# Kernel optimization log

Measured on AMD Instinct MI355X. Metric: run time of the kernel, lower is better.

Reference implementation:

```python
import jax, jax.numpy as jnp
import numpy as np
import math

CR = 16  # compress_ratio


def _head_mlp(x, W1, b1, W2, b2):
    # x: [..., NH, DH, CR]; per-head timm-style Mlp CR -> 4*CR -> 1 with exact GELU
    h = jax.nn.gelu(jnp.einsum('bgmnhk,nkf->bgmnhf', x, W1) + b1[:, None, :], approximate=False)
    return jnp.einsum('bgmnhf,nfo->bgmnho', h, W2) + b2[:, None, :]


def setup_inputs() -> dict:
    key = jax.random.key(0)
    ks = jax.random.split(key, 8)
    B, L, T, D, NH, OUT = 2, 256, 250, 1024, 16, 1024
    HID = 4 * CR
    mem = jax.random.normal(ks[0], (B, L * T + 1, D), jnp.float32)
    lm_emb = jax.random.normal(ks[1], (B, L, 1, D), jnp.float32)  # only shape is used
    dim_pe = jax.random.normal(ks[2], (CR, D), jnp.float32) * 0.02
    s1 = 1.0 / math.sqrt(CR)
    s2 = 1.0 / math.sqrt(HID)
    vW1 = jax.random.normal(ks[3], (NH, CR, HID), jnp.float32) * s1
    vb1 = jnp.zeros((NH, HID), jnp.float32)
    vW2 = jax.random.normal(ks[4], (NH, HID, 1), jnp.float32) * s2
    vb2 = jnp.zeros((NH, 1), jnp.float32)
    hW1 = jax.random.normal(ks[5], (NH, CR, HID), jnp.float32) * s1
    hb1 = jnp.zeros((NH, HID), jnp.float32)
    hW2 = jax.random.normal(ks[6], (NH, HID, 1), jnp.float32) * s2
    hb2 = jnp.zeros((NH, 1), jnp.float32)
    projW = jax.random.normal(ks[7], (OUT, D), jnp.float32) * (1.0 / math.sqrt(D))
    projb = jnp.zeros((OUT,), jnp.float32)
    return dict(mem=mem, lm_emb=lm_emb, dim_pe=dim_pe,
                vW1=vW1, vb1=vb1, vW2=vW2, vb2=vb2,
                hW1=hW1, hb1=hb1, hW2=hW2, hb2=hb2,
                projW=projW, projb=projb)


def reference(mem, lm_emb, dim_pe, vW1, vb1, vW2, vb2, hW1, hb1, hW2, hb2, projW, projb):
    B, L, _, D = lm_emb.shape
    NH = vW1.shape[0]
    DH = D // NH
    nonsense = mem[:, -1:]                                 # [B,1,D]
    x = mem[:, :-1].reshape(B, L, -1, D)                   # [B,L,T,D]
    T = x.shape[2]
    CL = L // CR
    # vertical compression over l-groups of CR
    v = jnp.transpose(x, (0, 2, 1, 3)).reshape(B, T, CL, CR, NH, DH)
    v = v + dim_pe.reshape(1, 1, 1, CR, NH, DH)
    v = jnp.transpose(v, (0, 1, 2, 4, 5, 3))               # [B,T,CL,NH,DH,CR]
    v = _head_mlp(v, vW1, vb1, vW2, vb2)[..., 0]           # [B,T,CL,NH,DH]
    v = v.reshape(B, T, CL, D)
    v = jnp.transpose(v, (0, 2, 1, 3))                     # [B,CL,T,D]
    # pad t to a multiple of CR with the 'nonsense' token
    pad_t = -(-T // CR) * CR
    pad = jnp.broadcast_to(nonsense.reshape(B, 1, 1, D), (B, CL, pad_t - T, D))
    v = jnp.concatenate([v, pad], axis=-2)                 # [B,CL,pad_t,D]
    # horizontal compression over t-groups of CR
    h = v.reshape(B, CL, pad_t // CR, CR, NH, DH)
    h = jnp.transpose(h, (0, 1, 2, 4, 5, 3))               # [B,CL,pad_t//CR,NH,DH,CR]
    h = _head_mlp(h, hW1, hb1, hW2, hb2)[..., 0]           # [B,CL,pad_t//CR,NH,DH]
    h = h.reshape(B, CL * (pad_t // CR), D)
    return h @ projW.T + projb
```

## Files before the change

kernel.cpp:

```cpp
#include <hip/hip_runtime.h>
#include <hip/hip_bf16.h>

#define B_ 2
#define L_ 256
#define T_ 250
#define D_ 1024
#define NH_ 16
#define DH_ 64
#define CRv_ 16
#define HID_ 64
#define CL_ 16
#define OUT_ 1024
#define MEMROWS_ 64001L

#define AS1 __attribute__((address_space(1)))
#define AS3 __attribute__((address_space(3)))

typedef __attribute__((ext_vector_type(2))) _Float16 h16x2;
typedef __attribute__((ext_vector_type(8))) _Float16 h16x8;
typedef __attribute__((ext_vector_type(4))) float f32x4;

__device__ __forceinline__ h16x2 cvt_pk(float lo, float hi) {
    return __builtin_bit_cast(h16x2, __builtin_amdgcn_cvt_pkrtz(lo, hi));
}
__device__ __forceinline__ unsigned cvt_pku(float lo, float hi) {
    return __builtin_bit_cast(unsigned, __builtin_amdgcn_cvt_pkrtz(lo, hi));
}

struct H4 { h16x2 a, b, c, d; };
__device__ __forceinline__ h16x8 packH4(h16x2 a, h16x2 b, h16x2 c, h16x2 d) {
    H4 h{a, b, c, d};
    return __builtin_bit_cast(h16x8, h);
}

__device__ __forceinline__ unsigned pk_fma(unsigned a, unsigned b, unsigned c) {
    unsigned d; asm("v_pk_fma_f16 %0, %1, %2, %3" : "=v"(d) : "v"(a), "v"(b), "v"(c)); return d;
}
__device__ __forceinline__ unsigned pk_mul(unsigned a, unsigned b) {
    unsigned d; asm("v_pk_mul_f16 %0, %1, %2" : "=v"(d) : "v"(a), "v"(b)); return d;
}
__device__ __forceinline__ unsigned pk_add(unsigned a, unsigned b) {
    unsigned d; asm("v_pk_add_f16 %0, %1, %2" : "=v"(d) : "v"(a), "v"(b)); return d;
}
__device__ __forceinline__ unsigned pk_max(unsigned a, unsigned b) {
    unsigned d; asm("v_pk_max_f16 %0, %1, %2" : "=v"(d) : "v"(a), "v"(b)); return d;
}
__device__ __forceinline__ unsigned pk_min(unsigned a, unsigned b) {
    unsigned d; asm("v_pk_min_f16 %0, %1, %2" : "=v"(d) : "v"(a), "v"(b)); return d;
}

struct GC { unsigned c0, c1, c2, c3, c4, clo, chi; };
__device__ __forceinline__ GC make_gc() {
    GC g;
    g.c0  = cvt_pku( 1.5957600f,   1.5957600f);
    g.c1  = cvt_pku(-1.0445624f,  -1.0445624f);
    g.c2  = cvt_pku( 0.5417632f,   0.5417632f);
    g.c3  = cvt_pku(-0.15817472f, -0.15817472f);
    g.c4  = cvt_pku( 0.018604288f, 0.018604288f);
    g.clo = cvt_pku(-1.75f, -1.75f);
    g.chi = cvt_pku( 1.75f,  1.75f);
    return g;
}

__device__ __forceinline__ void gelu_w2_asm(unsigned aH, unsigned w, unsigned& pacc, const GC& gc) {
    unsigned t = pk_min(pk_max(aH, gc.clo), gc.chi);
    unsigned s = pk_mul(t, t);
    unsigned p = pk_fma(gc.c4, s, gc.c3);
    p = pk_fma(p, s, gc.c2);
    p = pk_fma(p, s, gc.c1);
    p = pk_fma(p, s, gc.c0);
    unsigned e = pk_mul(t, p);
    unsigned g = pk_fma(aH, e, aH);
    pacc = pk_fma(g, w, pacc);
}

#define WAITV(n) asm volatile("s_waitcnt vmcnt(" #n ")" ::: "memory")
#define MEMBAR() asm volatile("" ::: "memory")

__global__ __launch_bounds__(512) void k_stage1(
    const float* __restrict__ mem, const float* __restrict__ dim_pe,
    const float* __restrict__ W1, const float* __restrict__ b1,
    const float* __restrict__ W2, const float* __restrict__ b2,
    _Float16* __restrict__ vbuf)
{
    extern __shared__ float stage[];

    const int blk   = blockIdx.x;
    const int dhalf = blk & 1;
    const int tch   = (blk >> 1) & 7;
    const int cl    = (blk >> 4) & 15;
    const int b     = blk >> 8;
    const int lane  = threadIdx.x & 63;
    const int wv    = threadIdx.x >> 6;
    const int nh    = dhalf * 8 + wv;
    const int g     = lane >> 4;
    const int fl    = lane & 15;
    const int kbase = (8 * g) & 15;
    const bool klive = (g < 2);

    const float* membase = mem + (long)b * MEMROWS_ * D_;
    _Float16* vrow = vbuf + (long)(b * CL_ + cl) * T_ * D_;
    const int t0   = tch * 31 + (tch < 2 ? tch : 2);
    const int tend = (tch < 2) ? 32 : 31;

    const GC gc = make_gc();

    h16x8 peq[4];
#pragma unroll
    for (int ct = 0; ct < 4; ++ct) {
        const int d0 = nh * DH_ + ct * 16 + fl;
        float p0 = dim_pe[(kbase + 0) * D_ + d0];
        float p1 = dim_pe[(kbase + 1) * D_ + d0];
        float p2 = dim_pe[(kbase + 2) * D_ + d0];
        float p3 = dim_pe[(kbase + 3) * D_ + d0];
        float p4 = dim_pe[(kbase + 4) * D_ + d0];
        float p5 = dim_pe[(kbase + 5) * D_ + d0];
        float p6 = dim_pe[(kbase + 6) * D_ + d0];
        float p7 = dim_pe[(kbase + 7) * D_ + d0];
        peq[ct] = packH4(cvt_pk(p0, p1), cvt_pk(p2, p3), cvt_pk(p4, p5), cvt_pk(p6, p7));
    }

    h16x8 bfragA[4];
    f32x4 ci[4];
    unsigned w2u[8];
#pragma unroll
    for (int cn = 0; cn < 4; ++cn) {
        h16x2 q[4];
#pragma unroll
        for (int jp = 0; jp < 4; ++jp) {
            float w0 = 0.5f * W1[(nh * CRv_ + kbase + 2 * jp + 0) * HID_ + cn * 16 + fl];
            float w1 = 0.5f * W1[(nh * CRv_ + kbase + 2 * jp + 1) * HID_ + cn * 16 + fl];
            q[jp] = cvt_pk(w0, w1);
        }
        bfragA[cn] = packH4(q[0], q[1], q[2], q[3]);
#pragma unroll
        for (int r = 0; r < 4; ++r) ci[cn][r] = 0.5f * b1[nh * HID_ + cn * 16 + 4 * g + r];
        w2u[2 * cn + 0] = cvt_pku(W2[nh * HID_ + cn * 16 + 4 * g + 0],
                                  W2[nh * HID_ + cn * 16 + 4 * g + 1]);
        w2u[2 * cn + 1] = cvt_pku(W2[nh * HID_ + cn * 16 + 4 * g + 2],
                                  W2[nh * HID_ + cn * 16 + 4 * g + 3]);
    }
    const float b2s = b2[nh];
    const unsigned b2p = cvt_pku(b2s, b2s);

    const int r0 = 2 * wv, r1 = 2 * wv + 1;
    const float* gp0 = membase + ((size_t)(cl * CRv_ + r0) * T_ + t0) * D_ + dhalf * 512 +   0 + lane * 4;
    const float* gp1 = membase + ((size_t)(cl * CRv_ + r0) * T_ + t0) * D_ + dhalf * 512 + 256 + lane * 4;
    const float* gp2 = membase + ((size_t)(cl * CRv_ + r1) * T_ + t0) * D_ + dhalf * 512 +   0 + lane * 4;
    const float* gp3 = membase + ((size_t)(cl * CRv_ + r1) * T_ + t0) * D_ + dhalf * 512 + 256 + lane * 4;

#define ISSUE(bf) do { \
    float* lb = stage + (bf) * 8192; \
    __builtin_amdgcn_global_load_lds((const AS1 void*)gp0, (AS3 void*)(lb + r0 * 512 +   0), 16, 0, 0); \
    __builtin_amdgcn_global_load_lds((const AS1 void*)gp1, (AS3 void*)(lb + r0 * 512 + 256), 16, 0, 0); \
    __builtin_amdgcn_global_load_lds((const AS1 void*)gp2, (AS3 void*)(lb + r1 * 512 +   0), 16, 0, 0); \
    __builtin_amdgcn_global_load_lds((const AS1 void*)gp3, (AS3 void*)(lb + r1 * 512 + 256), 16, 0, 0); \
    gp0 += D_; gp1 += D_; gp2 += D_; gp3 += D_; } while (0)

    ISSUE(0);

    for (int tt = 0; tt < tend; ++tt) {
        if (tt + 1 < tend) {
            ISSUE((tt + 1) & 1);
            if (tt == 0) WAITV(4); else WAITV(5);
        } else {
            WAITV(1);
        }
        __builtin_amdgcn_s_barrier();
        MEMBAR();

        const float* bufp = stage + (tt & 1) * 8192;
        float prl[4];
#pragma unroll
        for (int ct = 0; ct < 4; ++ct) {
            const int col = wv * 64 + ct * 16 + fl;
            float a0 = bufp[(kbase + 0) * 512 + col];
            float a1 = bufp[(kbase + 1) * 512 + col];
            float a2 = bufp[(kbase + 2) * 512 + col];
            float a3 = bufp[(kbase + 3) * 512 + col];
            float a4 = bufp[(kbase + 4) * 512 + col];
            float a5 = bufp[(kbase + 5) * 512 + col];
            float a6 = bufp[(kbase + 6) * 512 + col];
            float a7 = bufp[(kbase + 7) * 512 + col];
            h16x8 xq = packH4(cvt_pk(a0, a1), cvt_pk(a2, a3), cvt_pk(a4, a5), cvt_pk(a6, a7));
            h16x8 af = klive ? xq : peq[ct];

            f32x4 acc[4];
#pragma unroll
            for (int cn = 0; cn < 4; ++cn)
                acc[cn] = __builtin_amdgcn_mfma_f32_16x16x32_f16(bfragA[cn], af, ci[cn], 0, 0, 0);

            unsigned pc0 = 0u, pc1 = 0u;
#pragma unroll
            for (int cn = 0; cn < 4; ++cn) {
                unsigned a01 = cvt_pku(acc[cn][0], acc[cn][1]);
                unsigned a23 = cvt_pku(acc[cn][2], acc[cn][3]);
                gelu_w2_asm(a01, w2u[2 * cn + 0], pc0, gc);
                gelu_w2_asm(a23, w2u[2 * cn + 1], pc1, gc);
            }
            h16x2 P = __builtin_bit_cast(h16x2, pk_add(pc0, pc1));
            prl[ct] = (float)P[0] + (float)P[1];
        }

        unsigned A  = cvt_pku(prl[0], prl[1]);
        unsigned Bp = cvt_pku(prl[2], prl[3]);
        A  = pk_add(A,  (unsigned)__shfl_xor((int)A, 16));
        Bp = pk_add(Bp, (unsigned)__shfl_xor((int)Bp, 16));
        A  = pk_add(A,  (unsigned)__shfl_xor((int)A, 32));
        Bp = pk_add(Bp, (unsigned)__shfl_xor((int)Bp, 32));
        A  = pk_add(A, b2p);
        Bp = pk_add(Bp, b2p);
        unsigned sel = (g < 2) ? A : Bp;
        unsigned sh  = (g & 1) ? (sel >> 16) : sel;
        vrow[(size_t)(t0 + tt) * D_ + nh * DH_ + g * 16 + fl] =
            __builtin_bit_cast(_Float16, (unsigned short)sh);

        MEMBAR();
        __builtin_amdgcn_s_barrier();
        MEMBAR();
    }
#undef ISSUE
}

__global__ __launch_bounds__(256) void k_stage2(
    const _Float16* __restrict__ vbuf, const float* __restrict__ mem,
    const float* __restrict__ W1, const float* __restrict__ b1,
    const float* __restrict__ W2, const float* __restrict__ b2,
    _Float16* __restrict__ hbuf)
{
    const int blk = blockIdx.x;
    const int nhg = blk & 3;
    const int tc  = (blk >> 2) & 15;
    const int cl  = (blk >> 6) & 15;
    const int b   = blk >> 10;
    const int lane = threadIdx.x & 63;
    const int wv   = threadIdx.x >> 6;
    const int nh   = nhg * 4 + wv;
    const int g    = lane >> 4;
    const int fl   = lane & 15;
    const int kbase = (8 * g) & 15;
    const bool klive = (g < 2);

    const _Float16* vrow = vbuf + (long)(b * CL_ + cl) * T_ * D_;
    const float* nons = mem + ((long)b * MEMROWS_ + (long)L_ * T_) * D_;

    const GC gc = make_gc();

    h16x8 bfragA[4];
    f32x4 ci[4];
    unsigned w2u[8];
#pragma unroll
    for (int cn = 0; cn < 4; ++cn) {
        h16x2 q[4];
#pragma unroll
        for (int jp = 0; jp < 4; ++jp) {
            float w0 = 0.5f * W1[(nh * CRv_ + kbase + 2 * jp + 0) * HID_ + cn * 16 + fl];
            float w1 = 0.5f * W1[(nh * CRv_ + kbase + 2 * jp + 1) * HID_ + cn * 16 + fl];
            h16x2 qq = cvt_pk(w0, w1);
            if (!klive) { qq[0] = (_Float16)0.f; qq[1] = (_Float16)0.f; }
            q[jp] = qq;
        }
        bfragA[cn] = packH4(q[0], q[1], q[2], q[3]);
#pragma unroll
        for (int r = 0; r < 4; ++r) ci[cn][r] = 0.5f * b1[nh * HID_ + cn * 16 + 4 * g + r];
        w2u[2 * cn + 0] = cvt_pku(W2[nh * HID_ + cn * 16 + 4 * g + 0],
                                  W2[nh * HID_ + cn * 16 + 4 * g + 1]);
        w2u[2 * cn + 1] = cvt_pku(W2[nh * HID_ + cn * 16 + 4 * g + 2],
                                  W2[nh * HID_ + cn * 16 + 4 * g + 3]);
    }
    const float b2s = b2[nh];

#pragma unroll 1
    for (int ct = 0; ct < 4; ++ct) {
        const int d0 = nh * DH_ + ct * 16 + fl;
        const _Float16 nv = (_Float16)nons[d0];

        h16x2 q[4];
#pragma unroll
        for (int jp = 0; jp < 4; ++jp) {
            h16x2 qq;
#pragma unroll
            for (int e = 0; e < 2; ++e) {
                const int t   = tc * CRv_ + kbase + 2 * jp + e;
                const int tcl = (t < T_) ? t : (T_ - 1);
                _Float16 us = vrow[tcl * D_ + d0];
                qq[e] = (t < T_) ? us : nv;
            }
            q[jp] = qq;
        }
        h16x8 af = packH4(q[0], q[1], q[2], q[3]);

        f32x4 acc[4];
#pragma unroll
        for (int cn = 0; cn < 4; ++cn)
            acc[cn] = __builtin_amdgcn_mfma_f32_16x16x32_f16(bfragA[cn], af, ci[cn], 0, 0, 0);

        unsigned pc0 = 0u, pc1 = 0u;
#pragma unroll
        for (int cn = 0; cn < 4; ++cn) {
            unsigned a01 = cvt_pku(acc[cn][0], acc[cn][1]);
            unsigned a23 = cvt_pku(acc[cn][2], acc[cn][3]);
            gelu_w2_asm(a01, w2u[2 * cn + 0], pc0, gc);
            gelu_w2_asm(a23, w2u[2 * cn + 1], pc1, gc);
        }
        h16x2 P = __builtin_bit_cast(h16x2, pk_add(pc0, pc1));
        float pr = (float)P[0] + (float)P[1];
        pr += __shfl_xor(pr, 16);
        pr += __shfl_xor(pr, 32);

        if (g == 0)
            hbuf[(long)((b * CL_ + cl) * 16 + tc) * D_ + d0] = (_Float16)(pr + b2s);
    }
}

__global__ __launch_bounds__(256) void k_proj(
    const _Float16* __restrict__ H, const float* __restrict__ Wp,
    const float* __restrict__ bias, float* __restrict__ Cout)
{
    __shared__ _Float16 Ht[64][40];
    __shared__ _Float16 Wt[32][40];

    const int bn = blockIdx.x & 31;
    const int bm = blockIdx.x >> 5;
    const int tid = threadIdx.x;
    const int lane = tid & 63, wv = tid >> 6;
    const int g = lane >> 4, fl = lane & 15;
    const int m0 = bm * 64, n0 = bn * 32;

    const int hrow = tid >> 2, hko = (tid & 3) * 8;
    const int wrow = tid >> 3, wko = (tid & 7) * 4;

    const int nw  = (wv & 1) * 16;
    const int mwb = (wv >> 1) * 32;

    f32x4 acc[2] = {{0.f,0.f,0.f,0.f},{0.f,0.f,0.f,0.f}};

    for (int k0 = 0; k0 < 1024; k0 += 32) {
        uint4 hv = *reinterpret_cast<const uint4*>(&H[(size_t)(m0 + hrow) * OUT_ + k0 + hko]);
        *reinterpret_cast<uint4*>(&Ht[hrow][hko]) = hv;
        float4 wf = *reinterpret_cast<const float4*>(&Wp[(size_t)(n0 + wrow) * D_ + k0 + wko]);
        uint2 wu;
        wu.x = cvt_pku(wf.x, wf.y);
        wu.y = cvt_pku(wf.z, wf.w);
        *reinterpret_cast<uint2*>(&Wt[wrow][wko]) = wu;
        __syncthreads();

        h16x8 wfrag = *reinterpret_cast<const h16x8*>(&Wt[nw + fl][g * 8]);
        h16x8 hfrag0 = *reinterpret_cast<const h16x8*>(&Ht[mwb +  0 + fl][g * 8]);
        h16x8 hfrag1 = *reinterpret_cast<const h16x8*>(&Ht[mwb + 16 + fl][g * 8]);
        acc[0] = __builtin_amdgcn_mfma_f32_16x16x32_f16(hfrag0, wfrag, acc[0], 0, 0, 0);
        acc[1] = __builtin_amdgcn_mfma_f32_16x16x32_f16(hfrag1, wfrag, acc[1], 0, 0, 0);
        __syncthreads();
    }

    const int n = n0 + nw + fl;
    const float bv = bias[n];
#pragma unroll
    for (int mt = 0; mt < 2; ++mt) {
#pragma unroll
        for (int r = 0; r < 4; ++r) {
            const int m = m0 + mwb + mt * 16 + 4 * g + r;
            Cout[(size_t)m * OUT_ + n] = acc[mt][r] + bv;
        }
    }
}

extern "C" void kernel_launch(void* const* d_in, const int* in_sizes, int n_in,
                              void* d_out, int out_size, void* d_ws, size_t ws_size,
                              hipStream_t stream) {
    const float* mem    = (const float*)d_in[0];
    const float* dim_pe = (const float*)d_in[2];
    const float* vW1    = (const float*)d_in[3];
    const float* vb1    = (const float*)d_in[4];
    const float* vW2    = (const float*)d_in[5];
    const float* vb2    = (const float*)d_in[6];
    const float* hW1    = (const float*)d_in[7];
    const float* hb1    = (const float*)d_in[8];
    const float* hW2    = (const float*)d_in[9];
    const float* hb2    = (const float*)d_in[10];
    const float* projW  = (const float*)d_in[11];
    const float* projb  = (const float*)d_in[12];
    float* out = (float*)d_out;

    _Float16* vbuf = (_Float16*)d_ws;
    _Float16* hbuf = (_Float16*)((char*)d_ws + (size_t)B_ * CL_ * T_ * D_ * sizeof(_Float16));

    k_stage1<<<B_ * CL_ * 8 * 2, 512, 65536, stream>>>(mem, dim_pe, vW1, vb1, vW2, vb2, vbuf);
    k_stage2<<<B_ * CL_ * 16 * 4, 256, 0, stream>>>(vbuf, mem, hW1, hb1, hW2, hb2, hbuf);
    k_proj<<<256, 256, 0, stream>>>(hbuf, projW, projb, out);
}
```

Measured before the change: 183.8 us.

## Switch stage-1 head MLP to 32x32x16 MFMA and fold dim_pe add

```diff
diff --git a/kernel.cpp b/kernel.cpp
--- a/kernel.cpp
+++ b/kernel.cpp
@@ -19,6 +19,7 @@
 typedef __attribute__((ext_vector_type(2))) _Float16 h16x2;
 typedef __attribute__((ext_vector_type(8))) _Float16 h16x8;
 typedef __attribute__((ext_vector_type(4))) float f32x4;
+typedef __attribute__((ext_vector_type(16))) float f32x16;
 
 __device__ __forceinline__ h16x2 cvt_pk(float lo, float hi) {
     return __builtin_bit_cast(h16x2, __builtin_amdgcn_cvt_pkrtz(lo, hi));
@@ -31,6 +32,11 @@
 __device__ __forceinline__ h16x8 packH4(h16x2 a, h16x2 b, h16x2 c, h16x2 d) {
     H4 h{a, b, c, d};
     return __builtin_bit_cast(h16x8, h);
+}
+struct U4 { unsigned a, b, c, d; };
+__device__ __forceinline__ h16x8 packU4(unsigned a, unsigned b, unsigned c, unsigned d) {
+    U4 u{a, b, c, d};
+    return __builtin_bit_cast(h16x8, u);
 }
 
 __device__ __forceinline__ unsigned pk_fma(unsigned a, unsigned b, unsigned c) {
@@ -77,7 +83,7 @@
 #define WAITV(n) asm volatile("s_waitcnt vmcnt(" #n ")" ::: "memory")
 #define MEMBAR() asm volatile("" ::: "memory")
 
-__global__ __launch_bounds__(512) void k_stage1(
+__global__ __launch_bounds__(512, 4) void k_stage1(
     const float* __restrict__ mem, const float* __restrict__ dim_pe,
     const float* __restrict__ W1, const float* __restrict__ b1,
     const float* __restrict__ W2, const float* __restrict__ b2,
@@ -93,10 +99,8 @@
     const int lane  = threadIdx.x & 63;
     const int wv    = threadIdx.x >> 6;
     const int nh    = dhalf * 8 + wv;
-    const int g     = lane >> 4;
-    const int fl    = lane & 15;
-    const int kbase = (8 * g) & 15;
-    const bool klive = (g < 2);
+    const int h     = lane >> 5;
+    const int l31   = lane & 31;
 
     const float* membase = mem + (long)b * MEMROWS_ * D_;
     _Float16* vrow = vbuf + (long)(b * CL_ + cl) * T_ * D_;
@@ -105,43 +109,45 @@
 
     const GC gc = make_gc();
 
-    h16x8 peq[4];
-#pragma unroll
-    for (int ct = 0; ct < 4; ++ct) {
-        const int d0 = nh * DH_ + ct * 16 + fl;
-        float p0 = dim_pe[(kbase + 0) * D_ + d0];
-        float p1 = dim_pe[(kbase + 1) * D_ + d0];
-        float p2 = dim_pe[(kbase + 2) * D_ + d0];
-        float p3 = dim_pe[(kbase + 3) * D_ + d0];
-        float p4 = dim_pe[(kbase + 4) * D_ + d0];
-        float p5 = dim_pe[(kbase + 5) * D_ + d0];
-        float p6 = dim_pe[(kbase + 6) * D_ + d0];
-        float p7 = dim_pe[(kbase + 7) * D_ + d0];
-        peq[ct] = packH4(cvt_pk(p0, p1), cvt_pk(p2, p3), cvt_pk(p4, p5), cvt_pk(p6, p7));
-    }
-
-    h16x8 bfragA[4];
-    f32x4 ci[4];
-    unsigned w2u[8];
-#pragma unroll
-    for (int cn = 0; cn < 4; ++cn) {
+    h16x8 afrag[2];
+#pragma unroll
+    for (int fh = 0; fh < 2; ++fh) {
         h16x2 q[4];
 #pragma unroll
         for (int jp = 0; jp < 4; ++jp) {
-            float w0 = 0.5f * W1[(nh * CRv_ + kbase + 2 * jp + 0) * HID_ + cn * 16 + fl];
-            float w1 = 0.5f * W1[(nh * CRv_ + kbase + 2 * jp + 1) * HID_ + cn * 16 + fl];
+            float w0 = 0.5f * W1[(nh * CRv_ + 8 * h + 2 * jp + 0) * HID_ + fh * 32 + l31];
+            float w1 = 0.5f * W1[(nh * CRv_ + 8 * h + 2 * jp + 1) * HID_ + fh * 32 + l31];
             q[jp] = cvt_pk(w0, w1);
         }
-        bfragA[cn] = packH4(q[0], q[1], q[2], q[3]);
-#pragma unroll
-        for (int r = 0; r < 4; ++r) ci[cn][r] = 0.5f * b1[nh * HID_ + cn * 16 + 4 * g + r];
-        w2u[2 * cn + 0] = cvt_pku(W2[nh * HID_ + cn * 16 + 4 * g + 0],
-                                  W2[nh * HID_ + cn * 16 + 4 * g + 1]);
-        w2u[2 * cn + 1] = cvt_pku(W2[nh * HID_ + cn * 16 + 4 * g + 2],
-                                  W2[nh * HID_ + cn * 16 + 4 * g + 3]);
+        afrag[fh] = packH4(q[0], q[1], q[2], q[3]);
+    }
+
+    f32x16 ci[2];
+#pragma unroll
+    for (int fh = 0; fh < 2; ++fh)
+#pragma unroll
+        for (int r = 0; r < 16; ++r)
+            ci[fh][r] = 0.5f * b1[nh * HID_ + fh * 32 + (r & 3) + 8 * (r >> 2) + 4 * h];
+
+    unsigned w2u[2][8];
+#pragma unroll
+    for (int fh = 0; fh < 2; ++fh)
+#pragma unroll
+        for (int m = 0; m < 8; ++m) {
+            const int flo = ((2 * m) & 3) + 8 * (m >> 1) + 4 * h + fh * 32;
+            w2u[fh][m] = cvt_pku(W2[nh * HID_ + flo], W2[nh * HID_ + flo + 1]);
+        }
+
+    unsigned peq[2][4];
+#pragma unroll
+    for (int dh = 0; dh < 2; ++dh) {
+        const int d0 = nh * DH_ + dh * 32 + l31;
+#pragma unroll
+        for (int m = 0; m < 4; ++m)
+            peq[dh][m] = cvt_pku(dim_pe[(8 * h + 2 * m + 0) * D_ + d0],
+                                 dim_pe[(8 * h + 2 * m + 1) * D_ + d0]);
     }
     const float b2s = b2[nh];
-    const unsigned b2p = cvt_pku(b2s, b2s);
 
     const int r0 = 2 * wv, r1 = 2 * wv + 1;
     const float* gp0 = membase + ((size_t)(cl * CRv_ + r0) * T_ + t0) * D_ + dhalf * 512 +   0 + lane * 4;
@@ -170,50 +176,58 @@
         MEMBAR();
 
         const float* bufp = stage + (tt & 1) * 8192;
-        float prl[4];
-#pragma unroll
-        for (int ct = 0; ct < 4; ++ct) {
-            const int col = wv * 64 + ct * 16 + fl;
-            float a0 = bufp[(kbase + 0) * 512 + col];
-            float a1 = bufp[(kbase + 1) * 512 + col];
-            float a2 = bufp[(kbase + 2) * 512 + col];
-            float a3 = bufp[(kbase + 3) * 512 + col];
-            float a4 = bufp[(kbase + 4) * 512 + col];
-            float a5 = bufp[(kbase + 5) * 512 + col];
-            float a6 = bufp[(kbase + 6) * 512 + col];
-            float a7 = bufp[(kbase + 7) * 512 + col];
-            h16x8 xq = packH4(cvt_pk(a0, a1), cvt_pk(a2, a3), cvt_pk(a4, a5), cvt_pk(a6, a7));
-            h16x8 af = klive ? xq : peq[ct];
-
-            f32x4 acc[4];
-#pragma unroll
-            for (int cn = 0; cn < 4; ++cn)
-                acc[cn] = __builtin_amdgcn_mfma_f32_16x16x32_f16(bfragA[cn], af, ci[cn], 0, 0, 0);
-
-            unsigned pc0 = 0u, pc1 = 0u;
-#pragma unroll
-            for (int cn = 0; cn < 4; ++cn) {
-                unsigned a01 = cvt_pku(acc[cn][0], acc[cn][1]);
-                unsigned a23 = cvt_pku(acc[cn][2], acc[cn][3]);
-                gelu_w2_asm(a01, w2u[2 * cn + 0], pc0, gc);
-                gelu_w2_asm(a23, w2u[2 * cn + 1], pc1, gc);
+
+        h16x8 bfr[2];
+#pragma unroll
+        for (int dh = 0; dh < 2; ++dh) {
+            const int col = wv * 64 + dh * 32 + l31;
+            float x0 = bufp[(8 * h + 0) * 512 + col];
+            float x1 = bufp[(8 * h + 1) * 512 + col];
+            float x2 = bufp[(8 * h + 2) * 512 + col];
+            float x3 = bufp[(8 * h + 3) * 512 + col];
+            float x4 = bufp[(8 * h + 4) * 512 + col];
+            float x5 = bufp[(8 * h + 5) * 512 + col];
+            float x6 = bufp[(8 * h + 6) * 512 + col];
+            float x7 = bufp[(8 * h + 7) * 512 + col];
+            unsigned u0 = pk_add(cvt_pku(x0, x1), peq[dh][0]);
+            unsigned u1 = pk_add(cvt_pku(x2, x3), peq[dh][1]);
+            unsigned u2 = pk_add(cvt_pku(x4, x5), peq[dh][2]);
+            unsigned u3 = pk_add(cvt_pku(x6, x7), peq[dh][3]);
+            bfr[dh] = packU4(u0, u1, u2, u3);
+        }
+
+        unsigned p00 = 0u, p01 = 0u, p10 = 0u, p11 = 0u;
+        {
+            f32x16 a00 = __builtin_amdgcn_mfma_f32_32x32x16_f16(afrag[0], bfr[0], ci[0], 0, 0, 0);
+            f32x16 a01 = __builtin_amdgcn_mfma_f32_32x32x16_f16(afrag[0], bfr[1], ci[0], 0, 0, 0);
+#pragma unroll
+            for (int m = 0; m < 8; ++m) {
+                unsigned am0 = cvt_pku(a00[2 * m], a00[2 * m + 1]);
+                gelu_w2_asm(am0, w2u[0][m], p00, gc);
+                unsigned am1 = cvt_pku(a01[2 * m], a01[2 * m + 1]);
+                gelu_w2_asm(am1, w2u[0][m], p01, gc);
             }
-            h16x2 P = __builtin_bit_cast(h16x2, pk_add(pc0, pc1));
-            prl[ct] = (float)P[0] + (float)P[1];
-        }
-
-        unsigned A  = cvt_pku(prl[0], prl[1]);
-        unsigned Bp = cvt_pku(prl[2], prl[3]);
-        A  = pk_add(A,  (unsigned)__shfl_xor((int)A, 16));
-        Bp = pk_add(Bp, (unsigned)__shfl_xor((int)Bp, 16));
-        A  = pk_add(A,  (unsigned)__shfl_xor((int)A, 32));
-        Bp = pk_add(Bp, (unsigned)__shfl_xor((int)Bp, 32));
-        A  = pk_add(A, b2p);
-        Bp = pk_add(Bp, b2p);
-        unsigned sel = (g < 2) ? A : Bp;
-        unsigned sh  = (g & 1) ? (sel >> 16) : sel;
-        vrow[(size_t)(t0 + tt) * D_ + nh * DH_ + g * 16 + fl] =
-            __builtin_bit_cast(_Float16, (unsigned short)sh);
+        }
+        {
+            f32x16 a10 = __builtin_amdgcn_mfma_f32_32x32x16_f16(afrag[1], bfr[0], ci[1], 0, 0, 0);
+            f32x16 a11 = __builtin_amdgcn_mfma_f32_32x32x16_f16(afrag[1], bfr[1], ci[1], 0, 0, 0);
+#pragma unroll
+            for (int m = 0; m < 8; ++m) {
+                unsigned am0 = cvt_pku(a10[2 * m], a10[2 * m + 1]);
+                gelu_w2_asm(am0, w2u[1][m], p10, gc);
+                unsigned am1 = cvt_pku(a11[2 * m], a11[2 * m + 1]);
+                gelu_w2_asm(am1, w2u[1][m], p11, gc);
+            }
+        }
+
+        h16x2 pd0 = __builtin_bit_cast(h16x2, pk_add(p00, p10));
+        h16x2 pd1 = __builtin_bit_cast(h16x2, pk_add(p01, p11));
+        float o0 = (float)pd0[0] + (float)pd0[1];
+        float o1 = (float)pd1[0] + (float)pd1[1];
+        o0 += __shfl_xor(o0, 32);
+        o1 += __shfl_xor(o1, 32);
+        float ov = (h == 0) ? o0 : o1;
+        vrow[(size_t)(t0 + tt) * D_ + nh * DH_ + lane] = (_Float16)(ov + b2s);
 
         MEMBAR();
         __builtin_amdgcn_s_barrier();
```

New measurement: 167.0 us. 1.1x faster.
